# Kernel optimization log

Hardware: AMD Instinct MI355X
Metric: run time of the kernel (lower is better)

## Reference

```python
import jax, jax.numpy as jnp
import numpy as np

N_ATOM = 100000
N_BOND = 400000
N_GLOBAL = 5000
IN = 128
OUT = 128
HEADS = 2
NEG_SLOPE = 0.2
BN_EPS = 1e-5


def setup_inputs() -> dict:
    key = jax.random.key(0)
    ks = jax.random.split(key, 12)
    atom_feats = jax.random.normal(ks[0], (N_ATOM, IN), jnp.float32)
    bond_feats = jax.random.normal(ks[1], (N_BOND, IN), jnp.float32)
    global_feats = jax.random.normal(ks[2], (N_GLOBAL, IN), jnp.float32)
    W_atom = jax.random.normal(ks[3], (IN, OUT * HEADS), jnp.float32) * 0.05
    W_bond = jax.random.normal(ks[4], (IN, OUT * HEADS), jnp.float32) * 0.05
    W_global = jax.random.normal(ks[5], (IN, OUT * HEADS), jnp.float32) * 0.05
    attn_l = jax.random.normal(ks[6], (1, HEADS, OUT), jnp.float32) * 0.1
    attn_r = jax.random.normal(ks[7], (1, HEADS, OUT), jnp.float32) * 0.1
    bn_gamma = jnp.ones((OUT,), jnp.float32)
    bn_beta = jnp.zeros((OUT,), jnp.float32)
    bond_src = jax.random.randint(ks[8], (N_BOND,), 0, N_ATOM, jnp.int32)
    # ensure every atom appears as a bond destination at least once (DGL-like semantics)
    bond_dst = jnp.concatenate([
        jnp.arange(N_ATOM, dtype=jnp.int32),
        jax.random.randint(ks[9], (N_BOND - N_ATOM,), 0, N_ATOM, jnp.int32),
    ])
    g2a_src = jax.random.randint(ks[10], (N_ATOM,), 0, N_GLOBAL, jnp.int32)
    return dict(atom_feats=atom_feats, bond_feats=bond_feats, global_feats=global_feats,
                W_atom=W_atom, W_bond=W_bond, W_global=W_global,
                attn_l=attn_l, attn_r=attn_r, bn_gamma=bn_gamma, bn_beta=bn_beta,
                bond_src=bond_src, bond_dst=bond_dst, g2a_src=g2a_src)


def _fwd(atom_feats, bond_feats, global_feats, W_atom, W_bond, W_global,
         attn_l, attn_r, bn_gamma, bn_beta, bond_src, bond_dst, g2a_src):
    lrelu = lambda x: jax.nn.leaky_relu(x, NEG_SLOPE)
    # projections -> [*, H, D]
    h = (atom_feats @ W_atom).reshape(-1, HEADS, OUT)      # [N,H,D]
    e = (bond_feats @ W_bond).reshape(-1, HEADS, OUT)      # [E,H,D]
    u = (global_feats @ W_global).reshape(-1, HEADS, OUT)  # [G,H,D]
    er = (h * attn_r).sum(-1)    # [N,H]
    el_h = (h * attn_l).sum(-1)  # [N,H]
    el_e = (e * attn_l).sum(-1)  # [E,H]
    el_u = (u * attn_l).sum(-1)  # [G,H]
    er_dst = er[bond_dst]                      # [E,H]
    eh = lrelu(el_h[bond_src] + er_dst)        # bond: u_add_v
    ee = lrelu(el_e + er_dst)                  # bond: e_add_v
    eu = lrelu(el_u[g2a_src] + er)             # g2a: u_add_v (dst = arange(N))
    # numerically-stable edge softmax over both edge types per destination atom
    emax_b = jax.ops.segment_max(jnp.maximum(eh, ee), bond_dst, num_segments=N_ATOM)
    emax = jnp.maximum(emax_b, eu)             # [N,H]
    eh = jnp.exp(eh - emax[bond_dst])
    ee = jnp.exp(ee - emax[bond_dst])
    eu = jnp.exp(eu - emax)
    esum = jax.ops.segment_sum(eh + ee, bond_dst, num_segments=N_ATOM) + eu  # [N,H]
    esum_dst = esum[bond_dst]
    alpha_h = eh / esum_dst    # [E,H]
    alpha_e = ee / esum_dst
    alpha_u = eu / esum        # [N,H]
    msg = h[bond_src] * alpha_h[:, :, None] + e * alpha_e[:, :, None]  # [E,H,D]
    out = jax.ops.segment_sum(msg, bond_dst, num_segments=N_ATOM)
    out = out + u[g2a_src] * alpha_u[:, :, None]   # [N,H,D]
    hN = out.mean(axis=1)                           # mean over heads -> [N,D]
    # BatchNorm1d (training-mode batch stats, biased var)
    mean = hN.mean(axis=0)
    var = ((hN - mean) ** 2).mean(axis=0)
    hN = (hN - mean) * jax.lax.rsqrt(var + BN_EPS) * bn_gamma + bn_beta
    return jax.nn.relu(hN)


def reference(atom_feats, bond_feats, global_feats, W_atom, W_bond, W_global,
              attn_l, attn_r, bn_gamma, bn_beta, bond_src, bond_dst, g2a_src):
    return _fwd(atom_feats, bond_feats, global_feats, W_atom, W_bond, W_global,
                attn_l, attn_r, bn_gamma, bn_beta, bond_src, bond_dst, g2a_src)
```

## Files before the change

### kernel.cpp

```cpp
#include <hip/hip_runtime.h>
#include <hip/hip_bf16.h>

#define NA 100000
#define NB 400000
#define NG 5000
#define NEG 0.2f
#define KDIM 512
#define CAP 32
#define GEMM_BLKS 782
#define NA_PAD (GEMM_BLKS*128)
#define NROWS (NA+NB+NG)
#define KSC_BLKS 7891

typedef __attribute__((ext_vector_type(8))) short bf16x8;
typedef __attribute__((ext_vector_type(8))) unsigned short u16x8;
typedef __attribute__((ext_vector_type(4))) float f32x4;

__device__ __forceinline__ float lrelu(float x){ return x > 0.f ? x : NEG*x; }
__device__ __forceinline__ unsigned short f2bf(float f){
  unsigned u = __float_as_uint(f);
  u = (u + 0x7FFFu + ((u>>16)&1u)) >> 16;
  return (unsigned short)u;
}
__device__ __forceinline__ float bf2f(unsigned short s){
  return __uint_as_float(((unsigned)s) << 16);
}
__device__ __forceinline__ ushort2 pk2(float x, float y){
  __hip_bfloat162 t = __float22bfloat162_rn(make_float2(x, y));
  return *reinterpret_cast<ushort2*>(&t);
}
__device__ __forceinline__ void gl2lds16(const unsigned short* g, unsigned short* l){
  __builtin_amdgcn_global_load_lds(
      (const __attribute__((address_space(1))) unsigned int*)g,
      (__attribute__((address_space(3))) unsigned int*)l, 16, 0, 0);
}

__global__ void kW(const float* __restrict__ Wa, const float* __restrict__ Wb,
                   const float* __restrict__ Wg, const float* __restrict__ glob,
                   const float* __restrict__ al, const float* __restrict__ ar,
                   unsigned short* wTa, unsigned short* wTb, unsigned short* wTu,
                   unsigned short* WcT, unsigned short* P){
  int blk = blockIdx.x;
  int tid = threadIdx.x;
  if (blk == 0){
    int k = tid >> 1, h = tid & 1;
    const float* wa = Wa + k*256 + h*128;
    const float* wb = Wb + k*256 + h*128;
    const float* wg = Wg + k*256 + h*128;
    const float* pl = al + h*128;
    const float* pr = ar + h*128;
    float sa=0.f, sra=0.f, se=0.f, su=0.f;
    for (int d=0; d<128; ++d){
      float L = pl[d], R = pr[d];
      sa  += wa[d]*L;  sra += wa[d]*R;
      se  += wb[d]*L;  su  += wg[d]*L;
    }
    wTa[h*128 + k]     = f2bf(sa);
    wTa[(2+h)*128 + k] = f2bf(sra);
    wTb[h*128 + k]     = f2bf(se);
    wTu[h*128 + k]     = f2bf(su);
    for (int idx = tid; idx < 14*128; idx += 256){
      int c = 2 + (idx >> 7), k2 = idx & 127;
      wTb[c*128 + k2] = 0;
      wTu[c*128 + k2] = 0;
      if (c >= 4) wTa[c*128 + k2] = 0;
    }
  } else if (blk <= 256){
    int idx = (blk-1)*256 + tid;
    int c = idx / KDIM, j = idx % KDIM;
    int part = j >> 7, k = j & 127;
    const float* W = (part < 2) ? Wa : Wb;
    int h = part & 1;
    WcT[(size_t)c*KDIM + j] = f2bf(0.5f * W[k*256 + h*128 + c]);
  } else {
    __shared__ float gl[8][128];
    int g0 = (blk-257)*8;
    #pragma unroll
    for (int r=0;r<4;++r){
      int idx = r*256+tid;
      gl[idx>>7][idx&127] = glob[(size_t)(g0 + (idx>>7))*128 + (idx&127)];
    }
    __syncthreads();
    float acc[8];
    #pragma unroll
    for (int g=0;g<8;++g) acc[g]=0.f;
    for (int k=0;k<128;++k){
      float wv = Wg[k*256 + tid];
      #pragma unroll
      for (int g=0;g<8;++g) acc[g] += gl[g][k]*wv;
    }
    #pragma unroll
    for (int g=0;g<8;++g)
      P[(size_t)(g0+g)*256 + tid] = f2bf(0.5f*acc[g]);
  }
}

__global__ __launch_bounds__(256) void kSC(
    const float* __restrict__ atom, const float* __restrict__ bond,
    const float* __restrict__ glob,
    const unsigned short* __restrict__ wTa, const unsigned short* __restrict__ wTb,
    const unsigned short* __restrict__ wTu,
    float* __restrict__ el_h, float* __restrict__ er,
    float* __restrict__ el_e, float* __restrict__ el_u,
    unsigned short* __restrict__ atomB, unsigned short* __restrict__ bondB){
  __shared__ unsigned short lds[4][16*128];
  const int wid = threadIdx.x >> 6;
  const int l = threadIdx.x & 63;
  const long rowbase = ((long)blockIdx.x*4 + wid) * 16;

  const float* feats; const unsigned short* wT; unsigned short* fb;
  long r0; long nrows; int type;
  if (rowbase < NA){            feats = atom; wT = wTa; fb = atomB; r0 = rowbase;          nrows = NA; type = 0; }
  else if (rowbase < NA+NB){    feats = bond; wT = wTb; fb = bondB; r0 = rowbase-NA;       nrows = NB; type = 1; }
  else {                        feats = glob; wT = wTu; fb = nullptr; r0 = rowbase-(NA+NB); nrows = NG; type = 2; }

  bf16x8 bfrag[4];
  #pragma unroll
  for (int kk=0;kk<4;++kk)
    bfrag[kk] = *reinterpret_cast<const bf16x8*>(wT + (size_t)(l&15)*128 + kk*32 + (l>>4)*8);

  unsigned short* wlds = lds[wid];
  const int j = l & 15;
  const int rl0 = l >> 4;
  #pragma unroll
  for (int i=0;i<4;++i){
    int rl = rl0 + i*4;
    long gr = r0 + rl;
    long grc = gr < nrows ? gr : (nrows-1);
    const float* src = feats + grc*128 + j*8;
    float4 x0 = *reinterpret_cast<const float4*>(src);
    float4 x1 = *reinterpret_cast<const float4*>(src+4);
    u16x8 w;
    ushort2 c0 = pk2(x0.x, x0.y), c1 = pk2(x0.z, x0.w);
    ushort2 c2 = pk2(x1.x, x1.y), c3 = pk2(x1.z, x1.w);
    w[0]=c0.x; w[1]=c0.y; w[2]=c1.x; w[3]=c1.y;
    w[4]=c2.x; w[5]=c2.y; w[6]=c3.x; w[7]=c3.y;
    *reinterpret_cast<u16x8*>(&wlds[rl*128 + ((j ^ (rl&7))*8)]) = w;
    if (fb && gr < nrows)
      *reinterpret_cast<u16x8*>(fb + grc*128 + j*8) = w;
  }
  __syncthreads();

  f32x4 acc = (f32x4){0.f,0.f,0.f,0.f};
  const int arow = l & 15;
  #pragma unroll
  for (int kk=0;kk<4;++kk){
    int ch = (kk*4 + (l>>4)) ^ (arow & 7);
    bf16x8 a = *reinterpret_cast<const bf16x8*>(&wlds[arow*128 + ch*8]);
    acc = __builtin_amdgcn_mfma_f32_16x16x32_bf16(a, bfrag[kk], acc, 0, 0, 0);
  }

  const int col = l & 15;
  if (col < 4 && (type == 0 || col < 2)){
    #pragma unroll
    for (int i=0;i<4;++i){
      long gr = r0 + (l>>4)*4 + i;
      if (gr < nrows){
        float v = acc[i];
        if (type == 0){
          if (col < 2) el_h[2*gr + col] = v;
          else         er[2*gr + col-2] = v;
        } else if (type == 1){
          el_e[2*gr + col] = v;
        } else {
          el_u[2*gr + col] = v;
        }
      }
    }
  }
}

__global__ void k4_edgeexp(const int* __restrict__ bsrc, const int* __restrict__ bdst,
                           const float* __restrict__ el_h, const float* __restrict__ er,
                           const float* __restrict__ el_e,
                           int2* __restrict__ slot_bs, float4* __restrict__ slot_e,
                           int* __restrict__ cursor, float* __restrict__ esum){
  int b = blockIdx.x*256 + threadIdx.x;
  if (b >= NB) return;
  int s = bsrc[b], d = bdst[b];
  float2 elh = *reinterpret_cast<const float2*>(&el_h[2*s]);
  float2 erd = *reinterpret_cast<const float2*>(&er[2*d]);
  float2 ele = *reinterpret_cast<const float2*>(&el_e[2*b]);
  float a0 = __expf(lrelu(elh.x + erd.x));
  float a1 = __expf(lrelu(elh.y + erd.y));
  float b0 = __expf(lrelu(ele.x + erd.x));
  float b1 = __expf(lrelu(ele.y + erd.y));
  int pos = atomicAdd(&cursor[d], 1);
  if (pos < CAP){
    slot_bs[(size_t)d*CAP + pos] = make_int2(b, s);
    slot_e [(size_t)d*CAP + pos] = make_float4(a0, a1, b0, b1);
  }
  atomicAdd(&esum[2*d],   a0 + b0);
  atomicAdd(&esum[2*d+1], a1 + b1);
}

__global__ __launch_bounds__(256) void k8_agg(
    const unsigned short* __restrict__ atomB,
    const unsigned short* __restrict__ bondB,
    const int2* __restrict__ slot_bs, const float4* __restrict__ slot_e,
    const int* __restrict__ cursor, const float* __restrict__ esum,
    const float* __restrict__ el_u, const float* __restrict__ er,
    const int* __restrict__ g2a,
    unsigned short* __restrict__ X, float* __restrict__ guw){
  int n = blockIdx.x*4 + (threadIdx.x >> 6);
  int l = threadIdx.x & 63;
  int cc = cursor[n]; cc = cc > CAP ? CAP : cc;

  int g = g2a[n];
  float2 elu = *reinterpret_cast<const float2*>(&el_u[2*g]);
  float2 ern = *reinterpret_cast<const float2*>(&er[2*n]);
  float u0 = __expf(lrelu(elu.x + ern.x));
  float u1 = __expf(lrelu(elu.y + ern.y));
  float inv0 = 1.f / (esum[2*n]   + u0);
  float inv1 = 1.f / (esum[2*n+1] + u1);

  int sb = 0, ss = 0; float se0=0.f, se1=0.f, se2=0.f, se3=0.f;
  if (l < cc){
    int2 bs = slot_bs[(size_t)n*CAP + l];
    sb = bs.x; ss = bs.y;
    float4 e = slot_e[(size_t)n*CAP + l];
    se0 = e.x; se1 = e.y; se2 = e.z; se3 = e.w;
  }

  int grp = l >> 4;
  int li  = l & 15;
  float a0[8], a1[8], e0[8], e1[8];
  #pragma unroll
  for (int k=0;k<8;++k){ a0[k]=0.f; a1[k]=0.f; e0[k]=0.f; e1[k]=0.f; }

  for (int i=0; i<cc; i+=4){
    int j = i + grp;
    bool valid = j < cc;
    int bj = __shfl(sb, j & 31);
    int sj = __shfl(ss, j & 31);
    float ah0 = valid ? __shfl(se0, j & 31)*inv0 : 0.f;
    float ah1 = valid ? __shfl(se1, j & 31)*inv1 : 0.f;
    float ae0 = valid ? __shfl(se2, j & 31)*inv0 : 0.f;
    float ae1 = valid ? __shfl(se3, j & 31)*inv1 : 0.f;
    if (!valid){ bj = 0; sj = 0; }
    u16x8 xa = *reinterpret_cast<const u16x8*>(atomB + (size_t)sj*128 + 8*li);
    u16x8 xb = *reinterpret_cast<const u16x8*>(bondB + (size_t)bj*128 + 8*li);
    #pragma unroll
    for (int k=0;k<8;++k){
      float av = bf2f(xa[k]), bv = bf2f(xb[k]);
      a0[k] += ah0*av; a1[k] += ah1*av;
      e0[k] += ae0*bv; e1[k] += ae1*bv;
    }
  }
  #pragma unroll
  for (int k=0;k<8;++k){
    a0[k] += __shfl_xor(a0[k],16); a0[k] += __shfl_xor(a0[k],32);
    a1[k] += __shfl_xor(a1[k],16); a1[k] += __shfl_xor(a1[k],32);
    e0[k] += __shfl_xor(e0[k],16); e0[k] += __shfl_xor(e0[k],32);
    e1[k] += __shfl_xor(e1[k],16); e1[k] += __shfl_xor(e1[k],32);
  }
  u16x8 w;
  #pragma unroll
  for (int k=0;k<8;++k){
    float v = (grp==0) ? a0[k] : (grp==1) ? a1[k] : (grp==2) ? e0[k] : e1[k];
    w[k] = f2bf(v);
  }
  *reinterpret_cast<u16x8*>(X + (size_t)n*KDIM + grp*128 + 8*li) = w;
  if (l == 0){
    guw[2*n]   = u0*inv0;
    guw[2*n+1] = u1*inv1;
  }
}

__global__ __launch_bounds__(256) void k9_gemm(const unsigned short* __restrict__ X,
                                               const unsigned short* __restrict__ WcT,
                                               const int* __restrict__ g2a,
                                               const float* __restrict__ guw,
                                               const unsigned short* __restrict__ P,
                                               float* __restrict__ out,
                                               float* __restrict__ colsum,
                                               float* __restrict__ colsq){
  __shared__ unsigned short As[2][128*64];
  __shared__ unsigned short Bs[2][128*64];
  const int tid = threadIdx.x;
  const int l = tid & 63;
  const int w = tid >> 6;
  const int wr = w >> 1, wc = w & 1;
  const size_t brow0 = (size_t)blockIdx.x * 128;
  const unsigned short* Xblk = X + brow0 * KDIM;

  f32x4 acc[4][4];
  #pragma unroll
  for (int m=0;m<4;++m)
    #pragma unroll
    for (int n=0;n<4;++n) acc[m][n] = (f32x4){0.f,0.f,0.f,0.f};

  auto stage = [&](int buf, int kt){
    const unsigned short* Xk = Xblk + kt*64;
    const unsigned short* Wk = WcT  + kt*64;
    #pragma unroll
    for (int i=0;i<4;++i){
      int idx = i*256 + tid;
      int r = idx >> 3, ch = idx & 7;
      int kc = ch ^ (r & 7);
      gl2lds16(Xk + (size_t)r*KDIM + kc*8, &As[buf][idx*8]);
    }
    #pragma unroll
    for (int i=0;i<4;++i){
      int idx = i*256 + tid;
      int ccol = idx >> 3, ch = idx & 7;
      int kc = ch ^ (ccol & 7);
      gl2lds16(Wk + (size_t)ccol*KDIM + kc*8, &Bs[buf][idx*8]);
    }
  };

  auto compute = [&](int buf){
    #pragma unroll
    for (int kk=0; kk<2; ++kk){
      bf16x8 av[4], bv[4];
      #pragma unroll
      for (int m=0;m<4;++m){
        int row = wr*64 + m*16 + (l & 15);
        int slot = row*8 + ((kk*4 + (l>>4)) ^ (row & 7));
        av[m] = *reinterpret_cast<const bf16x8*>(&As[buf][slot*8]);
      }
      #pragma unroll
      for (int n=0;n<4;++n){
        int col = wc*64 + n*16 + (l & 15);
        int slot = col*8 + ((kk*4 + (l>>4)) ^ (col & 7));
        bv[n] = *reinterpret_cast<const bf16x8*>(&Bs[buf][slot*8]);
      }
      #pragma unroll
      for (int m=0;m<4;++m)
        #pragma unroll
        for (int n=0;n<4;++n)
          acc[m][n] = __builtin_amdgcn_mfma_f32_16x16x32_bf16(av[m], bv[n], acc[m][n], 0, 0, 0);
    }
  };

  stage(0, 0);
  asm volatile("s_waitcnt vmcnt(0)" ::: "memory");
  __syncthreads();
  for (int kt=0; kt<8; ++kt){
    int cur = kt & 1;
    if (kt < 7) stage(cur^1, kt+1);
    compute(cur);
    asm volatile("s_waitcnt vmcnt(0)" ::: "memory");
    __syncthreads();
  }

  float s[4] = {0.f,0.f,0.f,0.f};
  float q[4] = {0.f,0.f,0.f,0.f};
  #pragma unroll
  for (int m=0;m<4;++m){
    #pragma unroll
    for (int i=0;i<4;++i){
      size_t row = brow0 + wr*64 + m*16 + (l>>4)*4 + i;
      if (row < NA){
        int g = g2a[row];
        float2 au = *reinterpret_cast<const float2*>(&guw[2*row]);
        const unsigned short* Pg = P + (size_t)g*256;
        #pragma unroll
        for (int n=0;n<4;++n){
          int col = wc*64 + n*16 + (l & 15);
          float v = acc[m][n][i] + au.x*bf2f(Pg[col]) + au.y*bf2f(Pg[128+col]);
          out[row*128 + col] = v;
          s[n] += v; q[n] += v*v;
        }
      }
    }
  }
  #pragma unroll
  for (int n=0;n<4;++n){
    int col = wc*64 + n*16 + (l & 15);
    float sv = s[n], qv = q[n];
    sv += __shfl_xor(sv, 16); sv += __shfl_xor(sv, 32);
    qv += __shfl_xor(qv, 16); qv += __shfl_xor(qv, 32);
    if (l < 16){
      atomicAdd(&colsum[col], sv);
      atomicAdd(&colsq[col],  qv);
    }
  }
}

__global__ __launch_bounds__(256) void k11_bnrelu(float* __restrict__ out,
                            const float* __restrict__ colsum, const float* __restrict__ colsq,
                            const float* __restrict__ gamma, const float* __restrict__ beta){
  __shared__ float sc[128], sh[128];
  int t = threadIdx.x;
  if (t < 128){
    float mean = colsum[t] / (float)NA;
    float var = fmaxf(colsq[t] / (float)NA - mean*mean, 0.f);
    float s = gamma[t] * rsqrtf(var + 1e-5f);
    sc[t] = s;
    sh[t] = beta[t] - mean*s;
  }
  __syncthreads();
  int i = blockIdx.x*256 + t;
  float4 v = reinterpret_cast<float4*>(out)[i];
  int c0 = (i*4) & 127;
  v.x = fmaxf(0.f, v.x*sc[c0]   + sh[c0]);
  v.y = fmaxf(0.f, v.y*sc[c0+1] + sh[c0+1]);
  v.z = fmaxf(0.f, v.z*sc[c0+2] + sh[c0+2]);
  v.w = fmaxf(0.f, v.w*sc[c0+3] + sh[c0+3]);
  reinterpret_cast<float4*>(out)[i] = v;
}

extern "C" void kernel_launch(void* const* d_in, const int* in_sizes, int n_in,
                              void* d_out, int out_size, void* d_ws, size_t ws_size,
                              hipStream_t stream) {
  const float* atom = (const float*)d_in[0];
  const float* bond = (const float*)d_in[1];
  const float* glob = (const float*)d_in[2];
  const float* Wa   = (const float*)d_in[3];
  const float* Wb   = (const float*)d_in[4];
  const float* Wg   = (const float*)d_in[5];
  const float* al   = (const float*)d_in[6];
  const float* ar   = (const float*)d_in[7];
  const float* gamma= (const float*)d_in[8];
  const float* beta = (const float*)d_in[9];
  const int* bsrc   = (const int*)d_in[10];
  const int* bdst   = (const int*)d_in[11];
  const int* g2a    = (const int*)d_in[12];
  float* out = (float*)d_out;

  char* base = (char*)d_ws;
  size_t off = 0;
  auto carve = [&](size_t bytes)->void*{
    void* p = base + off;
    off = (off + bytes + 255) & ~(size_t)255;
    return p;
  };
  unsigned short* wTa = (unsigned short*)carve((size_t)16*128*2);
  unsigned short* wTb = (unsigned short*)carve((size_t)16*128*2);
  unsigned short* wTu = (unsigned short*)carve((size_t)16*128*2);
  unsigned short* WcT = (unsigned short*)carve((size_t)128*KDIM*2);
  unsigned short* P   = (unsigned short*)carve((size_t)NG*256*2);
  float* el_h = (float*)carve((size_t)NA*2*4);
  float* er   = (float*)carve((size_t)NA*2*4);
  float* el_e = (float*)carve((size_t)NB*2*4);
  float* el_u = (float*)carve((size_t)NG*2*4);
  float* guw  = (float*)carve((size_t)NA*2*4);
  char* zr = (char*)carve((size_t)NA*2*4 + (size_t)NA*4 + 256*4);
  float* esum   = (float*)(zr);
  int*   cursor = (int*)(zr + (size_t)NA*2*4);
  float* colsum = (float*)(zr + (size_t)NA*2*4 + (size_t)NA*4);
  float* colsq  = colsum + 128;
  size_t zbytes = (size_t)NA*2*4 + (size_t)NA*4 + 256*4;
  int2*   slot_bs = (int2*)carve((size_t)NA*CAP*8);
  float4* slot_e  = (float4*)carve((size_t)NA*CAP*16);
  unsigned short* atomB = (unsigned short*)carve((size_t)NA*128*2);
  unsigned short* bondB = (unsigned short*)carve((size_t)NB*128*2);
  unsigned short* X = (unsigned short*)carve((size_t)NA_PAD*KDIM*2);

  hipMemsetAsync(zr, 0, zbytes, stream);

  kW<<<882, 256, 0, stream>>>(Wa, Wb, Wg, glob, al, ar, wTa, wTb, wTu, WcT, P);

  kSC<<<KSC_BLKS, 256, 0, stream>>>(atom, bond, glob, wTa, wTb, wTu,
                                    el_h, er, el_e, el_u, atomB, bondB);

  k4_edgeexp<<<1563, 256, 0, stream>>>(bsrc, bdst, el_h, er, el_e,
                                       slot_bs, slot_e, cursor, esum);

  k8_agg<<<25000, 256, 0, stream>>>(atomB, bondB, slot_bs, slot_e, cursor, esum,
                                    el_u, er, g2a, X, guw);

  k9_gemm<<<GEMM_BLKS, 256, 0, stream>>>(X, WcT, g2a, guw, P, out, colsum, colsq);

  k11_bnrelu<<<12500, 256, 0, stream>>>(out, colsum, colsq, gamma, beta);
}
```

Before: 354.4 us.

## Fuse neighbor aggregation into the combine GEMM via LDS-resident tiles

Merges the edge aggregation kernel and the combine GEMM into one kernel. Each 512-thread block aggregates 128 atoms into a swizzled LDS tile, one half of K at a time (atom-feature phase, then bond-feature phase), and runs MFMA on it, so the large bf16 X intermediate and the guw buffer are never written to or read back from global memory. The weight operand is now read directly from global memory instead of being staged through LDS. Each 16-lane group walks edges serially with a one-ahead prefetch. The cost is lower parallelism: about 782 blocks do the gather work that 25000 blocks did before. There is also a 64KB LDS footprint per block, and agg and gemm alternate with no overlap between them.

```diff
diff --git a/kernel.cpp b/kernel.cpp
--- a/kernel.cpp
+++ b/kernel.cpp
@@ -8,8 +8,6 @@
 #define KDIM 512
 #define CAP 32
 #define GEMM_BLKS 782
-#define NA_PAD (GEMM_BLKS*128)
-#define NROWS (NA+NB+NG)
 #define KSC_BLKS 7891
 
 typedef __attribute__((ext_vector_type(8))) short bf16x8;
@@ -28,11 +26,6 @@
 __device__ __forceinline__ ushort2 pk2(float x, float y){
   __hip_bfloat162 t = __float22bfloat162_rn(make_float2(x, y));
   return *reinterpret_cast<ushort2*>(&t);
-}
-__device__ __forceinline__ void gl2lds16(const unsigned short* g, unsigned short* l){
-  __builtin_amdgcn_global_load_lds(
-      (const __attribute__((address_space(1))) unsigned int*)g,
-      (__attribute__((address_space(3))) unsigned int*)l, 16, 0, 0);
 }
 
 __global__ void kW(const float* __restrict__ Wa, const float* __restrict__ Wb,
@@ -194,181 +187,156 @@
   atomicAdd(&esum[2*d+1], a1 + b1);
 }
 
-__global__ __launch_bounds__(256) void k8_agg(
+__global__ __launch_bounds__(512, 4) void kFG(
     const unsigned short* __restrict__ atomB,
     const unsigned short* __restrict__ bondB,
     const int2* __restrict__ slot_bs, const float4* __restrict__ slot_e,
     const int* __restrict__ cursor, const float* __restrict__ esum,
     const float* __restrict__ el_u, const float* __restrict__ er,
     const int* __restrict__ g2a,
-    unsigned short* __restrict__ X, float* __restrict__ guw){
-  int n = blockIdx.x*4 + (threadIdx.x >> 6);
-  int l = threadIdx.x & 63;
-  int cc = cursor[n]; cc = cc > CAP ? CAP : cc;
-
-  int g = g2a[n];
-  float2 elu = *reinterpret_cast<const float2*>(&el_u[2*g]);
-  float2 ern = *reinterpret_cast<const float2*>(&er[2*n]);
-  float u0 = __expf(lrelu(elu.x + ern.x));
-  float u1 = __expf(lrelu(elu.y + ern.y));
-  float inv0 = 1.f / (esum[2*n]   + u0);
-  float inv1 = 1.f / (esum[2*n+1] + u1);
-
-  int sb = 0, ss = 0; float se0=0.f, se1=0.f, se2=0.f, se3=0.f;
-  if (l < cc){
-    int2 bs = slot_bs[(size_t)n*CAP + l];
-    sb = bs.x; ss = bs.y;
-    float4 e = slot_e[(size_t)n*CAP + l];
-    se0 = e.x; se1 = e.y; se2 = e.z; se3 = e.w;
-  }
-
-  int grp = l >> 4;
-  int li  = l & 15;
-  float a0[8], a1[8], e0[8], e1[8];
-  #pragma unroll
-  for (int k=0;k<8;++k){ a0[k]=0.f; a1[k]=0.f; e0[k]=0.f; e1[k]=0.f; }
-
-  for (int i=0; i<cc; i+=4){
-    int j = i + grp;
-    bool valid = j < cc;
-    int bj = __shfl(sb, j & 31);
-    int sj = __shfl(ss, j & 31);
-    float ah0 = valid ? __shfl(se0, j & 31)*inv0 : 0.f;
-    float ah1 = valid ? __shfl(se1, j & 31)*inv1 : 0.f;
-    float ae0 = valid ? __shfl(se2, j & 31)*inv0 : 0.f;
-    float ae1 = valid ? __shfl(se3, j & 31)*inv1 : 0.f;
-    if (!valid){ bj = 0; sj = 0; }
-    u16x8 xa = *reinterpret_cast<const u16x8*>(atomB + (size_t)sj*128 + 8*li);
-    u16x8 xb = *reinterpret_cast<const u16x8*>(bondB + (size_t)bj*128 + 8*li);
-    #pragma unroll
-    for (int k=0;k<8;++k){
-      float av = bf2f(xa[k]), bv = bf2f(xb[k]);
-      a0[k] += ah0*av; a1[k] += ah1*av;
-      e0[k] += ae0*bv; e1[k] += ae1*bv;
-    }
-  }
-  #pragma unroll
-  for (int k=0;k<8;++k){
-    a0[k] += __shfl_xor(a0[k],16); a0[k] += __shfl_xor(a0[k],32);
-    a1[k] += __shfl_xor(a1[k],16); a1[k] += __shfl_xor(a1[k],32);
-    e0[k] += __shfl_xor(e0[k],16); e0[k] += __shfl_xor(e0[k],32);
-    e1[k] += __shfl_xor(e1[k],16); e1[k] += __shfl_xor(e1[k],32);
-  }
-  u16x8 w;
-  #pragma unroll
-  for (int k=0;k<8;++k){
-    float v = (grp==0) ? a0[k] : (grp==1) ? a1[k] : (grp==2) ? e0[k] : e1[k];
-    w[k] = f2bf(v);
-  }
-  *reinterpret_cast<u16x8*>(X + (size_t)n*KDIM + grp*128 + 8*li) = w;
-  if (l == 0){
-    guw[2*n]   = u0*inv0;
-    guw[2*n+1] = u1*inv1;
-  }
-}
-
-__global__ __launch_bounds__(256) void k9_gemm(const unsigned short* __restrict__ X,
-                                               const unsigned short* __restrict__ WcT,
-                                               const int* __restrict__ g2a,
-                                               const float* __restrict__ guw,
-                                               const unsigned short* __restrict__ P,
-                                               float* __restrict__ out,
-                                               float* __restrict__ colsum,
-                                               float* __restrict__ colsq){
-  __shared__ unsigned short As[2][128*64];
-  __shared__ unsigned short Bs[2][128*64];
+    const unsigned short* __restrict__ WcT,
+    const unsigned short* __restrict__ P,
+    float* __restrict__ out, float* __restrict__ colsum, float* __restrict__ colsq){
+  __shared__ unsigned short XA[128*256];
+  __shared__ float au_s[128][2];
   const int tid = threadIdx.x;
-  const int l = tid & 63;
+  const int l  = tid & 63;
+  const int li = tid & 15;
+  const int gid = tid >> 4;
   const int w = tid >> 6;
-  const int wr = w >> 1, wc = w & 1;
-  const size_t brow0 = (size_t)blockIdx.x * 128;
-  const unsigned short* Xblk = X + brow0 * KDIM;
-
-  f32x4 acc[4][4];
+  const int wr = w >> 2, wc = w & 3;
+  const int gb = l & 48;
+  const int n0 = blockIdx.x * 128;
+
+  f32x4 acc[4][2];
   #pragma unroll
   for (int m=0;m<4;++m)
     #pragma unroll
-    for (int n=0;n<4;++n) acc[m][n] = (f32x4){0.f,0.f,0.f,0.f};
-
-  auto stage = [&](int buf, int kt){
-    const unsigned short* Xk = Xblk + kt*64;
-    const unsigned short* Wk = WcT  + kt*64;
-    #pragma unroll
-    for (int i=0;i<4;++i){
-      int idx = i*256 + tid;
-      int r = idx >> 3, ch = idx & 7;
-      int kc = ch ^ (r & 7);
-      gl2lds16(Xk + (size_t)r*KDIM + kc*8, &As[buf][idx*8]);
-    }
-    #pragma unroll
-    for (int i=0;i<4;++i){
-      int idx = i*256 + tid;
-      int ccol = idx >> 3, ch = idx & 7;
-      int kc = ch ^ (ccol & 7);
-      gl2lds16(Wk + (size_t)ccol*KDIM + kc*8, &Bs[buf][idx*8]);
+    for (int nf=0;nf<2;++nf) acc[m][nf] = (f32x4){0.f,0.f,0.f,0.f};
+
+  auto agg = [&](int phase){
+    for (int t=0; t<4; ++t){
+      int ln = gid + t*32;
+      int n = n0 + ln;
+      float a0[8], a1[8];
+      #pragma unroll
+      for (int k2=0;k2<8;++k2){ a0[k2]=0.f; a1[k2]=0.f; }
+      int cc = 0; float iv0=0.f, iv1=0.f;
+      if (n < NA){
+        cc = cursor[n]; cc = cc > CAP ? CAP : cc;
+        int g = g2a[n];
+        float2 elu = *reinterpret_cast<const float2*>(&el_u[2*g]);
+        float2 ern = *reinterpret_cast<const float2*>(&er[2*n]);
+        float u0 = __expf(lrelu(elu.x + ern.x));
+        float u1 = __expf(lrelu(elu.y + ern.y));
+        iv0 = 1.f/(esum[2*n]   + u0);
+        iv1 = 1.f/(esum[2*n+1] + u1);
+        if (phase==0 && li==0){ au_s[ln][0]=u0*iv0; au_s[ln][1]=u1*iv1; }
+      }
+      int idxA=0, idxB=0; float w0A=0.f,w1A=0.f,w0B=0.f,w1B=0.f;
+      if (li < cc){
+        int2 bs = slot_bs[(size_t)n*CAP + li];
+        float4 e = slot_e[(size_t)n*CAP + li];
+        idxA = phase ? bs.x : bs.y;
+        w0A = phase ? e.z : e.x;
+        w1A = phase ? e.w : e.y;
+      }
+      if (li+16 < cc){
+        int2 bs = slot_bs[(size_t)n*CAP + li+16];
+        float4 e = slot_e[(size_t)n*CAP + li+16];
+        idxB = phase ? bs.x : bs.y;
+        w0B = phase ? e.z : e.x;
+        w1B = phase ? e.w : e.y;
+      }
+      const unsigned short* tbl = phase ? bondB : atomB;
+      if (cc > 0){
+        int i0 = __shfl(idxA, gb);
+        u16x8 xr = *reinterpret_cast<const u16x8*>(tbl + (size_t)i0*128 + li*8);
+        for (int j=0; j<cc; ++j){
+          int jn = j+1;
+          u16x8 xn = xr;
+          if (jn < cc){
+            int sl2 = gb + (jn & 15);
+            int ij = (jn < 16) ? __shfl(idxA, sl2) : __shfl(idxB, sl2);
+            xn = *reinterpret_cast<const u16x8*>(tbl + (size_t)ij*128 + li*8);
+          }
+          int sl = gb + (j & 15);
+          float c0 = ((j < 16) ? __shfl(w0A, sl) : __shfl(w0B, sl)) * iv0;
+          float c1 = ((j < 16) ? __shfl(w1A, sl) : __shfl(w1B, sl)) * iv1;
+          #pragma unroll
+          for (int k2=0;k2<8;++k2){
+            float v = bf2f(xr[k2]);
+            a0[k2] += c0*v; a1[k2] += c1*v;
+          }
+          xr = xn;
+        }
+      }
+      u16x8 o0, o1;
+      #pragma unroll
+      for (int k2=0;k2<8;++k2){ o0[k2]=f2bf(a0[k2]); o1[k2]=f2bf(a1[k2]); }
+      *reinterpret_cast<u16x8*>(&XA[ln*256 + ((li     ) ^ (ln&7))*8]) = o0;
+      *reinterpret_cast<u16x8*>(&XA[ln*256 + ((16+li  ) ^ (ln&7))*8]) = o1;
     }
   };
 
-  auto compute = [&](int buf){
-    #pragma unroll
-    for (int kk=0; kk<2; ++kk){
-      bf16x8 av[4], bv[4];
+  auto gemm = [&](int phase){
+    #pragma unroll
+    for (int ks=0; ks<8; ++ks){
+      bf16x8 av[4], bv[2];
       #pragma unroll
       for (int m=0;m<4;++m){
-        int row = wr*64 + m*16 + (l & 15);
-        int slot = row*8 + ((kk*4 + (l>>4)) ^ (row & 7));
-        av[m] = *reinterpret_cast<const bf16x8*>(&As[buf][slot*8]);
-      }
-      #pragma unroll
-      for (int n=0;n<4;++n){
-        int col = wc*64 + n*16 + (l & 15);
-        int slot = col*8 + ((kk*4 + (l>>4)) ^ (col & 7));
-        bv[n] = *reinterpret_cast<const bf16x8*>(&Bs[buf][slot*8]);
+        int row = wr*64 + m*16 + (l&15);
+        int ch = (ks*4 + (l>>4)) ^ (row&7);
+        av[m] = *reinterpret_cast<const bf16x8*>(&XA[row*256 + ch*8]);
+      }
+      #pragma unroll
+      for (int nf=0;nf<2;++nf){
+        int col = wc*32 + nf*16 + (l&15);
+        bv[nf] = *reinterpret_cast<const bf16x8*>(
+            WcT + (size_t)col*KDIM + phase*256 + ks*32 + (l>>4)*8);
       }
       #pragma unroll
       for (int m=0;m<4;++m)
         #pragma unroll
-        for (int n=0;n<4;++n)
-          acc[m][n] = __builtin_amdgcn_mfma_f32_16x16x32_bf16(av[m], bv[n], acc[m][n], 0, 0, 0);
+        for (int nf=0;nf<2;++nf)
+          acc[m][nf] = __builtin_amdgcn_mfma_f32_16x16x32_bf16(av[m], bv[nf], acc[m][nf], 0, 0, 0);
     }
   };
 
-  stage(0, 0);
-  asm volatile("s_waitcnt vmcnt(0)" ::: "memory");
+  agg(0);
   __syncthreads();
-  for (int kt=0; kt<8; ++kt){
-    int cur = kt & 1;
-    if (kt < 7) stage(cur^1, kt+1);
-    compute(cur);
-    asm volatile("s_waitcnt vmcnt(0)" ::: "memory");
-    __syncthreads();
-  }
-
-  float s[4] = {0.f,0.f,0.f,0.f};
-  float q[4] = {0.f,0.f,0.f,0.f};
+  gemm(0);
+  __syncthreads();
+  agg(1);
+  __syncthreads();
+  gemm(1);
+
+  float s[2] = {0.f,0.f};
+  float q[2] = {0.f,0.f};
   #pragma unroll
   for (int m=0;m<4;++m){
     #pragma unroll
     for (int i=0;i<4;++i){
-      size_t row = brow0 + wr*64 + m*16 + (l>>4)*4 + i;
+      int row_l = wr*64 + m*16 + (l>>4)*4 + i;
+      size_t row = (size_t)n0 + row_l;
       if (row < NA){
+        float aux = au_s[row_l][0], auy = au_s[row_l][1];
         int g = g2a[row];
-        float2 au = *reinterpret_cast<const float2*>(&guw[2*row]);
         const unsigned short* Pg = P + (size_t)g*256;
         #pragma unroll
-        for (int n=0;n<4;++n){
-          int col = wc*64 + n*16 + (l & 15);
-          float v = acc[m][n][i] + au.x*bf2f(Pg[col]) + au.y*bf2f(Pg[128+col]);
+        for (int nf=0;nf<2;++nf){
+          int col = wc*32 + nf*16 + (l&15);
+          float v = acc[m][nf][i] + aux*bf2f(Pg[col]) + auy*bf2f(Pg[128+col]);
           out[row*128 + col] = v;
-          s[n] += v; q[n] += v*v;
+          s[nf] += v; q[nf] += v*v;
         }
       }
     }
   }
   #pragma unroll
-  for (int n=0;n<4;++n){
-    int col = wc*64 + n*16 + (l & 15);
-    float sv = s[n], qv = q[n];
+  for (int nf=0;nf<2;++nf){
+    int col = wc*32 + nf*16 + (l&15);
+    float sv = s[nf], qv = q[nf];
     sv += __shfl_xor(sv, 16); sv += __shfl_xor(sv, 32);
     qv += __shfl_xor(qv, 16); qv += __shfl_xor(qv, 32);
     if (l < 16){
@@ -435,7 +403,6 @@
   float* er   = (float*)carve((size_t)NA*2*4);
   float* el_e = (float*)carve((size_t)NB*2*4);
   float* el_u = (float*)carve((size_t)NG*2*4);
-  float* guw  = (float*)carve((size_t)NA*2*4);
   char* zr = (char*)carve((size_t)NA*2*4 + (size_t)NA*4 + 256*4);
   float* esum   = (float*)(zr);
   int*   cursor = (int*)(zr + (size_t)NA*2*4);
@@ -446,7 +413,6 @@
   float4* slot_e  = (float4*)carve((size_t)NA*CAP*16);
   unsigned short* atomB = (unsigned short*)carve((size_t)NA*128*2);
   unsigned short* bondB = (unsigned short*)carve((size_t)NB*128*2);
-  unsigned short* X = (unsigned short*)carve((size_t)NA_PAD*KDIM*2);
 
   hipMemsetAsync(zr, 0, zbytes, stream);
 
@@ -458,10 +424,8 @@
   k4_edgeexp<<<1563, 256, 0, stream>>>(bsrc, bdst, el_h, er, el_e,
                                        slot_bs, slot_e, cursor, esum);
 
-  k8_agg<<<25000, 256, 0, stream>>>(atomB, bondB, slot_bs, slot_e, cursor, esum,
-                                    el_u, er, g2a, X, guw);
-
-  k9_gemm<<<GEMM_BLKS, 256, 0, stream>>>(X, WcT, g2a, guw, P, out, colsum, colsq);
+  kFG<<<GEMM_BLKS, 512, 0, stream>>>(atomB, bondB, slot_bs, slot_e, cursor, esum,
+                                     el_u, er, g2a, WcT, P, out, colsum, colsq);
 
   k11_bnrelu<<<12500, 256, 0, stream>>>(out, colsum, colsq, gamma, beta);
 }
```

Measured after the change: 324.1 us. 1.09x faster.
